# Kernel tuning notes

Hardware: AMD Instinct MI355X
Metric: run time of the kernel (lower is better)

The kernel has to match this reference:

```python
import jax, jax.numpy as jnp
import numpy as np

H = 8            # num_heads
WIN = 128        # num_windows (sliding-window half-width)
B, T, C = 2, 4096, 512


def setup_inputs() -> dict:
    key = jax.random.key(0)
    k1, k2, k3 = jax.random.split(key, 3)
    x = jax.random.normal(k1, (B, T, C), dtype=jnp.float32)
    W_qkv = jax.random.normal(k2, (C, 3 * C), dtype=jnp.float32) * (C ** -0.5)
    W_out = jax.random.normal(k3, (C, C), dtype=jnp.float32) * (C ** -0.5)
    b_out = jnp.zeros((C,), dtype=jnp.float32)
    return {"x": x, "W_qkv": W_qkv, "W_out": W_out, "b_out": b_out}


def reference(x, W_qkv, W_out, b_out):
    Bx, Tx, Cx = x.shape
    hd = Cx // H
    scale = hd ** -0.5
    # qkv projection -> [B, T, 3, H, hd]
    qkv = (x @ W_qkv).reshape(Bx, Tx, 3, H, hd)
    q, k, v = qkv[:, :, 0], qkv[:, :, 1], qkv[:, :, 2]  # each [B, T, H, hd]
    # attention scores [B, H, T, T]
    scores = jnp.einsum('bihd,bjhd->bhij', q, k) * scale
    idx = jnp.arange(Tx)
    band = jnp.abs(idx[:, None] - idx[None, :]) <= WIN  # [T, T] bool
    scores = jnp.where(band[None, None], scores, jnp.float32(-jnp.inf))
    attn = jax.nn.softmax(scores, axis=-1)
    # dropout is identity in eval mode (p handled by config; omitted)
    out = jnp.einsum('bhij,bjhd->bihd', attn, v).reshape(Bx, Tx, Cx)
    return out @ W_out + b_out
```

## Files before the change

kernel.cpp:

```cpp
#include <hip/hip_runtime.h>
#include <stdint.h>

typedef unsigned short ushort_t;
typedef __attribute__((ext_vector_type(8))) __bf16 bf16x8;
typedef __attribute__((ext_vector_type(8))) unsigned short ushortx8;
typedef __attribute__((ext_vector_type(4))) float floatx4;
typedef __attribute__((ext_vector_type(4))) unsigned int uint4v;

__device__ inline ushort_t f2bf(float f) {
  union { float f; unsigned u; } v; v.f = f;
  unsigned r = v.u + 0x7FFFu + ((v.u >> 16) & 1u);
  return (ushort_t)(r >> 16);
}

__device__ inline floatx4 mfma16(bf16x8 a, bf16x8 b, floatx4 c) {
  return __builtin_amdgcn_mfma_f32_16x16x32_bf16(a, b, c, 0, 0, 0);
}

__device__ inline void gload_lds16(const ushort_t* g, ushort_t* l) {
  __builtin_amdgcn_global_load_lds((__attribute__((address_space(1))) void*)(void*)(g),
                                   (__attribute__((address_space(3))) void*)(l),
                                   16, 0, 0);
}

__global__ __launch_bounds__(256)
void k_prep(const float* __restrict__ x, ushort_t* __restrict__ xb,
            const float* __restrict__ Wqkv, ushort_t* __restrict__ wqkvT,
            const float* __restrict__ Wout, ushort_t* __restrict__ woutT) {
  int bx = blockIdx.x, tid = threadIdx.x;
  if (bx < 4096) {
    int i = (bx * 256 + tid) * 4;
    float4 v = *(const float4*)(x + i);
    ushort4 o;
    o.x = f2bf(v.x); o.y = f2bf(v.y); o.z = f2bf(v.z); o.w = f2bf(v.w);
    *(ushort4*)(xb + i) = o;
    return;
  }
  __shared__ float tile[32][33];
  const float* src; ushort_t* dst; int N, id;
  if (bx < 4096 + 768) { id = bx - 4096; src = Wqkv; dst = wqkvT; N = 1536; }
  else                 { id = bx - 4864; src = Wout; dst = woutT; N = 512;  }
  int k0 = (id & 15) * 32, n0 = (id >> 4) * 32;
  int c = tid & 31, r0 = tid >> 5;
#pragma unroll
  for (int i = 0; i < 4; ++i) {
    int r = r0 + i * 8;
    tile[r][c] = src[(size_t)(k0 + r) * N + n0 + c];
  }
  __syncthreads();
#pragma unroll
  for (int i = 0; i < 4; ++i) {
    int r = r0 + i * 8;
    dst[(size_t)(n0 + r) * 512 + k0 + c] = f2bf(tile[c][r]);
  }
}

template <int EPI, int MT>
__global__ __launch_bounds__(256)
void k_gemm_bt(const ushort_t* __restrict__ A, const ushort_t* __restrict__ Bt,
               ushort_t* __restrict__ qd, ushort_t* __restrict__ kd, ushort_t* __restrict__ vd,
               float* __restrict__ outf, const float* __restrict__ bias) {
  constexpr int ABLK = MT / 16;
  constexpr int AISS = ABLK * 2;
  constexpr int TOT  = AISS + 16;
  constexpr int PER  = TOT / 4;
  constexpr int IT   = MT / 32;
  __shared__ __align__(16) ushort_t As[ABLK * 1024];
  __shared__ __align__(16) ushort_t Bs[8 * 1024];
  const int tid = threadIdx.x;
  const int w = tid >> 6, l = tid & 63;
  const int lr = l & 15, lq = l >> 4;
  const int m0 = blockIdx.x * MT, n0 = blockIdx.y * 128;
  const int wm = w >> 1, wn = w & 1;

  floatx4 acc[IT][4];
#pragma unroll
  for (int i = 0; i < IT; ++i)
#pragma unroll
    for (int j = 0; j < 4; ++j) acc[i][j] = (floatx4)0.0f;

  for (int k0 = 0; k0 < 512; k0 += 64) {
#pragma unroll
    for (int i = 0; i < PER; ++i) {
      int idx = w * PER + i;
      if (idx < AISS) {
        int blk = idx >> 1, half = idx & 1;
        gload_lds16(A + (size_t)(m0 + blk * 16 + lr) * 512 + k0 + half * 32 + lq * 8,
                    &As[blk * 1024 + half * 512]);
      } else {
        int j = idx - AISS, blk = j >> 1, half = j & 1;
        gload_lds16(Bt + (size_t)(n0 + blk * 16 + lr) * 512 + k0 + half * 32 + lq * 8,
                    &Bs[blk * 1024 + half * 512]);
      }
    }
    __syncthreads();
#pragma unroll
    for (int half = 0; half < 2; ++half) {
      bf16x8 af[IT], bfr[4];
#pragma unroll
      for (int i = 0; i < IT; ++i)
        af[i] = *(const bf16x8*)&As[(wm * IT + i) * 1024 + half * 512 + l * 8];
#pragma unroll
      for (int j = 0; j < 4; ++j)
        bfr[j] = *(const bf16x8*)&Bs[(wn * 4 + j) * 1024 + half * 512 + l * 8];
#pragma unroll
      for (int i = 0; i < IT; ++i)
#pragma unroll
        for (int j = 0; j < 4; ++j) acc[i][j] = mfma16(af[i], bfr[j], acc[i][j]);
    }
    __syncthreads();
  }

#pragma unroll
  for (int i = 0; i < IT; ++i) {
#pragma unroll
    for (int j = 0; j < 4; ++j) {
      int n = n0 + wn * 64 + j * 16 + lr;
      if (EPI == 0) {
        int which = n >> 9, h = (n >> 6) & 7, d = n & 63;
        ushort_t* dst = (which == 0) ? qd : (which == 1) ? kd : vd;
#pragma unroll
        for (int r = 0; r < 4; ++r) {
          int m = m0 + wm * (IT * 16) + i * 16 + lq * 4 + r;
          int b = m >> 12, t = m & 4095;
          dst[(((size_t)(b * 8 + h)) * 4096 + t) * 64 + d] = f2bf(acc[i][j][r]);
        }
      } else {
        float bv = bias[n];
#pragma unroll
        for (int r = 0; r < 4; ++r) {
          int m = m0 + wm * (IT * 16) + i * 16 + lq * 4 + r;
          outf[(size_t)m * 512 + n] = acc[i][j][r] + bv;
        }
      }
    }
  }
}

__global__ __launch_bounds__(256) void k_transpose_v(const ushort_t* __restrict__ v,
                                                     ushort_t* __restrict__ vt) {
  __shared__ __align__(16) ushort_t lt[64][72];
  int tid = threadIdx.x, w = tid >> 6, l = tid & 63;
  int bh = blockIdx.y, t0 = blockIdx.x * 64;
  int row = w * 16 + (l & 15), ch = (l >> 4) * 16;
  const ushort_t* src = v + ((size_t)bh * 4096 + t0 + row) * 64 + ch;
  *(ushortx8*)&lt[row][ch] = *(const ushortx8*)src;
  *(ushortx8*)&lt[row][ch + 8] = *(const ushortx8*)(src + 8);
  __syncthreads();
  ushortx8 o0, o1;
#pragma unroll
  for (int i = 0; i < 8; ++i) o0[i] = lt[w * 16 + i][l];
#pragma unroll
  for (int i = 0; i < 8; ++i) o1[i] = lt[w * 16 + 8 + i][l];
  ushort_t* dst = vt + ((size_t)bh * 64 + l) * 4096 + t0 + w * 16;
  *(ushortx8*)dst = o0;
  *(ushortx8*)(dst + 8) = o1;
}

__global__ __launch_bounds__(256)
void k_attn(const ushort_t* __restrict__ qa, const ushort_t* __restrict__ ka,
            const ushort_t* __restrict__ vta, ushort_t* __restrict__ ao) {
  __shared__ __align__(16) ushort_t Vs[40 * 512];
  const int tid = threadIdx.x, w = tid >> 6, l = tid & 63;
  const int lr = l & 15, lq = l >> 4;
  const int bh = blockIdx.y, qt0 = blockIdx.x * 64;
  const int qrow = qt0 + w * 16;

  const ushort_t* vbase = vta + (size_t)bh * 64 * 4096;
#pragma unroll
  for (int i = 0; i < 10; ++i) {
    int t = w * 10 + i;
    int kt2 = t >> 2, nt = t & 3;
    int d = nt * 16 + lr;
    int key = qt0 - 128 + kt2 * 32 + lq * 8;
    key = min(max(key, 0), 4088);
    gload_lds16(vbase + (size_t)d * 4096 + key, &Vs[t * 512]);
  }

  const ushort_t* qp = qa + ((size_t)bh * 4096 + qrow + lr) * 64 + lq * 8;
  bf16x8 qf0 = *(const bf16x8*)qp;
  bf16x8 qf1 = *(const bf16x8*)(qp + 32);

  const float C = 0.125f * 1.4426950408889634f;
  uint2 pk[18];
  pk[17].x = 0u; pk[17].y = 0u;
  float ps = 0.f;
#pragma unroll
  for (int kt = 0; kt < 17; ++kt) {
    int kb = qrow - 128 + kt * 16;
    int kc = min(max(kb + lr, 0), 4095);
    const ushort_t* kp = ka + ((size_t)bh * 4096 + kc) * 64 + lq * 8;
    bf16x8 kf0 = *(const bf16x8*)kp;
    bf16x8 kf1 = *(const bf16x8*)(kp + 32);
    floatx4 s = (floatx4)0.0f;
    s = mfma16(kf0, qf0, s);
    s = mfma16(kf1, qf1, s);
    float p[4];
#pragma unroll
    for (int r = 0; r < 4; ++r) {
      int r_rel = kt * 16 + lq * 4 + r;
      int kj = qrow - 128 + r_rel;
      bool ok = (kj >= 0) && (kj < 4096) && (r_rel >= lr) && (r_rel - lr <= 256);
      float e = ok ? exp2f(s[r] * C) : 0.f;
      ps += e;
      p[r] = e;
    }
    pk[kt].x = (unsigned)f2bf(p[0]) | ((unsigned)f2bf(p[1]) << 16);
    pk[kt].y = (unsigned)f2bf(p[2]) | ((unsigned)f2bf(p[3]) << 16);
  }

  ps += __shfl_xor(ps, 16, 64);
  ps += __shfl_xor(ps, 32, 64);
  float inv = __builtin_amdgcn_rcpf(ps);

  __syncthreads();

  floatx4 oacc[4];
#pragma unroll
  for (int nt = 0; nt < 4; ++nt) oacc[nt] = (floatx4)0.0f;
  const int srcA = ((l >> 4) & 1) * 32 + lr;
  const int srcB = srcA + 16;
  const bool selhi = (l & 32) != 0;

#pragma unroll
  for (int kk = 0; kk < 9; ++kk) {
    unsigned e0 = __shfl(pk[2 * kk].x, srcA, 64);
    unsigned e1 = __shfl(pk[2 * kk].y, srcA, 64);
    unsigned e2 = __shfl(pk[2 * kk].x, srcB, 64);
    unsigned e3 = __shfl(pk[2 * kk].y, srcB, 64);
    unsigned o0 = __shfl(pk[2 * kk + 1].x, srcA, 64);
    unsigned o1 = __shfl(pk[2 * kk + 1].y, srcA, 64);
    unsigned o2 = __shfl(pk[2 * kk + 1].x, srcB, 64);
    unsigned o3 = __shfl(pk[2 * kk + 1].y, srcB, 64);
    union { uint4v u; bf16x8 b; } pu;
    pu.u[0] = selhi ? o0 : e0;
    pu.u[1] = selhi ? o1 : e1;
    pu.u[2] = selhi ? o2 : e2;
    pu.u[3] = selhi ? o3 : e3;

    int keyrel = w * 16 + kk * 32 + lq * 8;
    keyrel = min(keyrel, 312);
    int kt2 = keyrel >> 5, seg = (keyrel >> 3) & 3;
    const ushort_t* vsp = &Vs[kt2 * 2048 + seg * 128 + lr * 8];
#pragma unroll
    for (int nt = 0; nt < 4; ++nt) {
      bf16x8 vf = *(const bf16x8*)(vsp + nt * 512);
      oacc[nt] = mfma16(pu.b, vf, oacc[nt]);
    }
  }

  float invr[4];
#pragma unroll
  for (int r = 0; r < 4; ++r) invr[r] = __shfl(inv, lq * 4 + r, 64);

  int b = bh >> 3, h = bh & 7;
#pragma unroll
  for (int nt = 0; nt < 4; ++nt)
#pragma unroll
    for (int r = 0; r < 4; ++r) {
      int t = qrow + lq * 4 + r;
      int col = h * 64 + nt * 16 + lr;
      ao[((size_t)(b * 4096 + t)) * 512 + col] = f2bf(oacc[nt][r] * invr[r]);
    }
}

extern "C" void kernel_launch(void* const* d_in, const int* in_sizes, int n_in,
                              void* d_out, int out_size, void* d_ws, size_t ws_size,
                              hipStream_t stream) {
  const float* x    = (const float*)d_in[0];
  const float* Wqkv = (const float*)d_in[1];
  const float* Wout = (const float*)d_in[2];
  const float* bout = (const float*)d_in[3];
  float* out = (float*)d_out;
  char* ws = (char*)d_ws;
  const size_t MB = 1024 * 1024;

  ushort_t* xb    = (ushort_t*)(ws);
  ushort_t* wqkvT = (ushort_t*)(ws + 8 * MB);
  ushort_t* woutT = (ushort_t*)(ws + 9 * MB + MB/2);
  ushort_t* q     = (ushort_t*)(ws + 10 * MB);
  ushort_t* k     = (ushort_t*)(ws + 18 * MB);
  ushort_t* v     = (ushort_t*)(ws + 26 * MB);
  ushort_t* vt    = (ushort_t*)(ws + 34 * MB);
  ushort_t* ao    = xb;

  k_prep<<<5120, 256, 0, stream>>>(x, xb, Wqkv, wqkvT, Wout, woutT);
  k_gemm_bt<0, 128><<<dim3(64, 12), 256, 0, stream>>>(xb, wqkvT, q, k, v, nullptr, nullptr);
  k_transpose_v<<<dim3(64, 16), 256, 0, stream>>>(v, vt);
  k_attn<<<dim3(64, 16), 256, 0, stream>>>(q, k, vt, ao);
  k_gemm_bt<1, 64><<<dim3(128, 4), 256, 0, stream>>>(ao, woutT, nullptr, nullptr, nullptr, out, bout);
}
```

Before: 156.7 us.

## Fuse V transpose into QKV GEMM epilogue, stage K in LDS, coalesce outputs

The QKV GEMM epilogue now stages its tile through LDS and writes Q/K with 16-byte vector stores. It writes V directly in transposed layout, which removes the separate transpose kernel and the intermediate V buffer. The attention kernel loads its K window into shared memory with async global-to-LDS copies, then reuses the same buffer for V. Attention and output-projection epilogues also go through LDS so their global stores are coalesced. In exchange there are extra barriers, more LDS use and serialized K/V staging in attention.

Measured after the change: 143.8 us. 8.2% less time.

```diff
diff --git a/kernel.cpp b/kernel.cpp
--- a/kernel.cpp
+++ b/kernel.cpp
@@ -55,40 +55,35 @@
   }
 }
 
-template <int EPI, int MT>
 __global__ __launch_bounds__(256)
-void k_gemm_bt(const ushort_t* __restrict__ A, const ushort_t* __restrict__ Bt,
-               ushort_t* __restrict__ qd, ushort_t* __restrict__ kd, ushort_t* __restrict__ vd,
-               float* __restrict__ outf, const float* __restrict__ bias) {
-  constexpr int ABLK = MT / 16;
-  constexpr int AISS = ABLK * 2;
-  constexpr int TOT  = AISS + 16;
-  constexpr int PER  = TOT / 4;
-  constexpr int IT   = MT / 32;
-  __shared__ __align__(16) ushort_t As[ABLK * 1024];
-  __shared__ __align__(16) ushort_t Bs[8 * 1024];
+void k_gemm1(const ushort_t* __restrict__ A, const ushort_t* __restrict__ Bt,
+             ushort_t* __restrict__ qd, ushort_t* __restrict__ kd,
+             ushort_t* __restrict__ vtd) {
+  __shared__ __align__(16) ushort_t smem[17408];
+  ushort_t* As = smem;
+  ushort_t* Bs = smem + 8192;
   const int tid = threadIdx.x;
   const int w = tid >> 6, l = tid & 63;
   const int lr = l & 15, lq = l >> 4;
-  const int m0 = blockIdx.x * MT, n0 = blockIdx.y * 128;
+  const int m0 = blockIdx.x * 128, n0 = blockIdx.y * 128;
   const int wm = w >> 1, wn = w & 1;
 
-  floatx4 acc[IT][4];
-#pragma unroll
-  for (int i = 0; i < IT; ++i)
+  floatx4 acc[4][4];
+#pragma unroll
+  for (int i = 0; i < 4; ++i)
 #pragma unroll
     for (int j = 0; j < 4; ++j) acc[i][j] = (floatx4)0.0f;
 
   for (int k0 = 0; k0 < 512; k0 += 64) {
 #pragma unroll
-    for (int i = 0; i < PER; ++i) {
-      int idx = w * PER + i;
-      if (idx < AISS) {
+    for (int i = 0; i < 8; ++i) {
+      int idx = w * 8 + i;
+      if (idx < 16) {
         int blk = idx >> 1, half = idx & 1;
         gload_lds16(A + (size_t)(m0 + blk * 16 + lr) * 512 + k0 + half * 32 + lq * 8,
                     &As[blk * 1024 + half * 512]);
       } else {
-        int j = idx - AISS, blk = j >> 1, half = j & 1;
+        int j = idx - 16, blk = j >> 1, half = j & 1;
         gload_lds16(Bt + (size_t)(n0 + blk * 16 + lr) * 512 + k0 + half * 32 + lq * 8,
                     &Bs[blk * 1024 + half * 512]);
       }
@@ -96,102 +91,176 @@
     __syncthreads();
 #pragma unroll
     for (int half = 0; half < 2; ++half) {
-      bf16x8 af[IT], bfr[4];
-#pragma unroll
-      for (int i = 0; i < IT; ++i)
-        af[i] = *(const bf16x8*)&As[(wm * IT + i) * 1024 + half * 512 + l * 8];
+      bf16x8 af[4], bfr[4];
+#pragma unroll
+      for (int i = 0; i < 4; ++i)
+        af[i] = *(const bf16x8*)&As[(wm * 4 + i) * 1024 + half * 512 + l * 8];
 #pragma unroll
       for (int j = 0; j < 4; ++j)
         bfr[j] = *(const bf16x8*)&Bs[(wn * 4 + j) * 1024 + half * 512 + l * 8];
 #pragma unroll
-      for (int i = 0; i < IT; ++i)
+      for (int i = 0; i < 4; ++i)
 #pragma unroll
         for (int j = 0; j < 4; ++j) acc[i][j] = mfma16(af[i], bfr[j], acc[i][j]);
     }
     __syncthreads();
   }
 
-#pragma unroll
-  for (int i = 0; i < IT; ++i) {
+  if (blockIdx.y < 8) {
+#pragma unroll
+    for (int i = 0; i < 4; ++i)
+#pragma unroll
+      for (int j = 0; j < 4; ++j) {
+        int col = wn * 64 + j * 16 + lr;
+#pragma unroll
+        for (int r = 0; r < 4; ++r) {
+          int row = wm * 64 + i * 16 + lq * 4 + r;
+          smem[row * 136 + col] = f2bf(acc[i][j][r]);
+        }
+      }
+    __syncthreads();
+#pragma unroll
+    for (int p = 0; p < 8; ++p) {
+      int row = p * 16 + (tid >> 4), c8 = (tid & 15) * 8;
+      ushortx8 vv = *(const ushortx8*)&smem[row * 136 + c8];
+      int n = n0 + c8;
+      ushort_t* dst = (n >> 9) ? kd : qd;
+      int h = (n >> 6) & 7, d = n & 63;
+      int m = m0 + row, b = m >> 12, t = m & 4095;
+      *(ushortx8*)&dst[(((size_t)(b * 8 + h)) * 4096 + t) * 64 + d] = vv;
+    }
+  } else {
+#pragma unroll
+    for (int i = 0; i < 4; ++i)
+#pragma unroll
+      for (int j = 0; j < 4; ++j) {
+        int dcol = wn * 64 + j * 16 + lr;
+        int trow = wm * 64 + i * 16 + lq * 4;
+        ushort4 pv;
+        pv.x = f2bf(acc[i][j][0]); pv.y = f2bf(acc[i][j][1]);
+        pv.z = f2bf(acc[i][j][2]); pv.w = f2bf(acc[i][j][3]);
+        *(ushort4*)&smem[dcol * 136 + trow] = pv;
+      }
+    __syncthreads();
+#pragma unroll
+    for (int p = 0; p < 8; ++p) {
+      int row = p * 16 + (tid >> 4), c8 = (tid & 15) * 8;
+      ushortx8 vv = *(const ushortx8*)&smem[row * 136 + c8];
+      int n = n0 + row, h = (n >> 6) & 7, d = n & 63;
+      int m = m0 + c8, b = m >> 12, t = m & 4095;
+      *(ushortx8*)&vtd[(((size_t)(b * 8 + h)) * 64 + d) * 4096 + t] = vv;
+    }
+  }
+}
+
+__global__ __launch_bounds__(256)
+void k_gemm2(const ushort_t* __restrict__ A, const ushort_t* __restrict__ Bt,
+             float* __restrict__ outf, const float* __restrict__ bias) {
+  __shared__ __align__(16) char smemc[33792];
+  ushort_t* As = (ushort_t*)smemc;
+  ushort_t* Bs = (ushort_t*)(smemc + 8192);
+  float* Cs = (float*)smemc;
+  const int tid = threadIdx.x;
+  const int w = tid >> 6, l = tid & 63;
+  const int lr = l & 15, lq = l >> 4;
+  const int m0 = blockIdx.x * 64, n0 = blockIdx.y * 128;
+  const int wm = w >> 1, wn = w & 1;
+
+  floatx4 acc[2][4];
+#pragma unroll
+  for (int i = 0; i < 2; ++i)
+#pragma unroll
+    for (int j = 0; j < 4; ++j) acc[i][j] = (floatx4)0.0f;
+
+  for (int k0 = 0; k0 < 512; k0 += 64) {
+#pragma unroll
+    for (int i = 0; i < 6; ++i) {
+      int idx = w * 6 + i;
+      if (idx < 8) {
+        int blk = idx >> 1, half = idx & 1;
+        gload_lds16(A + (size_t)(m0 + blk * 16 + lr) * 512 + k0 + half * 32 + lq * 8,
+                    &As[blk * 1024 + half * 512]);
+      } else {
+        int j = idx - 8, blk = j >> 1, half = j & 1;
+        gload_lds16(Bt + (size_t)(n0 + blk * 16 + lr) * 512 + k0 + half * 32 + lq * 8,
+                    &Bs[blk * 1024 + half * 512]);
+      }
+    }
+    __syncthreads();
+#pragma unroll
+    for (int half = 0; half < 2; ++half) {
+      bf16x8 af[2], bfr[4];
+#pragma unroll
+      for (int i = 0; i < 2; ++i)
+        af[i] = *(const bf16x8*)&As[(wm * 2 + i) * 1024 + half * 512 + l * 8];
+#pragma unroll
+      for (int j = 0; j < 4; ++j)
+        bfr[j] = *(const bf16x8*)&Bs[(wn * 4 + j) * 1024 + half * 512 + l * 8];
+#pragma unroll
+      for (int i = 0; i < 2; ++i)
+#pragma unroll
+        for (int j = 0; j < 4; ++j) acc[i][j] = mfma16(af[i], bfr[j], acc[i][j]);
+    }
+    __syncthreads();
+  }
+
+#pragma unroll
+  for (int i = 0; i < 2; ++i)
 #pragma unroll
     for (int j = 0; j < 4; ++j) {
-      int n = n0 + wn * 64 + j * 16 + lr;
-      if (EPI == 0) {
-        int which = n >> 9, h = (n >> 6) & 7, d = n & 63;
-        ushort_t* dst = (which == 0) ? qd : (which == 1) ? kd : vd;
-#pragma unroll
-        for (int r = 0; r < 4; ++r) {
-          int m = m0 + wm * (IT * 16) + i * 16 + lq * 4 + r;
-          int b = m >> 12, t = m & 4095;
-          dst[(((size_t)(b * 8 + h)) * 4096 + t) * 64 + d] = f2bf(acc[i][j][r]);
-        }
-      } else {
-        float bv = bias[n];
-#pragma unroll
-        for (int r = 0; r < 4; ++r) {
-          int m = m0 + wm * (IT * 16) + i * 16 + lq * 4 + r;
-          outf[(size_t)m * 512 + n] = acc[i][j][r] + bv;
-        }
-      }
-    }
-  }
-}
-
-__global__ __launch_bounds__(256) void k_transpose_v(const ushort_t* __restrict__ v,
-                                                     ushort_t* __restrict__ vt) {
-  __shared__ __align__(16) ushort_t lt[64][72];
-  int tid = threadIdx.x, w = tid >> 6, l = tid & 63;
-  int bh = blockIdx.y, t0 = blockIdx.x * 64;
-  int row = w * 16 + (l & 15), ch = (l >> 4) * 16;
-  const ushort_t* src = v + ((size_t)bh * 4096 + t0 + row) * 64 + ch;
-  *(ushortx8*)&lt[row][ch] = *(const ushortx8*)src;
-  *(ushortx8*)&lt[row][ch + 8] = *(const ushortx8*)(src + 8);
-  __syncthreads();
-  ushortx8 o0, o1;
-#pragma unroll
-  for (int i = 0; i < 8; ++i) o0[i] = lt[w * 16 + i][l];
-#pragma unroll
-  for (int i = 0; i < 8; ++i) o1[i] = lt[w * 16 + 8 + i][l];
-  ushort_t* dst = vt + ((size_t)bh * 64 + l) * 4096 + t0 + w * 16;
-  *(ushortx8*)dst = o0;
-  *(ushortx8*)(dst + 8) = o1;
+      int col = wn * 64 + j * 16 + lr;
+      float bv = bias[n0 + col];
+#pragma unroll
+      for (int r = 0; r < 4; ++r) {
+        int row = wm * 32 + i * 16 + lq * 4 + r;
+        Cs[row * 132 + col] = acc[i][j][r] + bv;
+      }
+    }
+  __syncthreads();
+#pragma unroll
+  for (int p = 0; p < 4; ++p) {
+    int row = p * 16 + (tid >> 4), c = (tid & 15) * 8;
+    float4 v0 = *(const float4*)&Cs[row * 132 + c];
+    float4 v1 = *(const float4*)&Cs[row * 132 + c + 4];
+    float* op = &outf[(size_t)(m0 + row) * 512 + n0 + c];
+    *(float4*)op = v0;
+    *(float4*)(op + 4) = v1;
+  }
 }
 
 __global__ __launch_bounds__(256)
 void k_attn(const ushort_t* __restrict__ qa, const ushort_t* __restrict__ ka,
             const ushort_t* __restrict__ vta, ushort_t* __restrict__ ao) {
-  __shared__ __align__(16) ushort_t Vs[40 * 512];
+  __shared__ __align__(16) ushort_t S[20 * 1024];
   const int tid = threadIdx.x, w = tid >> 6, l = tid & 63;
   const int lr = l & 15, lq = l >> 4;
   const int bh = blockIdx.y, qt0 = blockIdx.x * 64;
   const int qrow = qt0 + w * 16;
 
-  const ushort_t* vbase = vta + (size_t)bh * 64 * 4096;
+  const ushort_t* kbase = ka + (size_t)bh * 4096 * 64;
 #pragma unroll
   for (int i = 0; i < 10; ++i) {
-    int t = w * 10 + i;
-    int kt2 = t >> 2, nt = t & 3;
-    int d = nt * 16 + lr;
-    int key = qt0 - 128 + kt2 * 32 + lq * 8;
-    key = min(max(key, 0), 4088);
-    gload_lds16(vbase + (size_t)d * 4096 + key, &Vs[t * 512]);
+    int idx = w * 10 + i, blk = idx >> 1, half = idx & 1;
+    int row = qt0 - 128 + blk * 16 + lr;
+    row = min(max(row, 0), 4095);
+    gload_lds16(kbase + (size_t)row * 64 + half * 32 + lq * 8, &S[blk * 1024 + half * 512]);
   }
 
   const ushort_t* qp = qa + ((size_t)bh * 4096 + qrow + lr) * 64 + lq * 8;
   bf16x8 qf0 = *(const bf16x8*)qp;
   bf16x8 qf1 = *(const bf16x8*)(qp + 32);
 
-  const float C = 0.125f * 1.4426950408889634f;
+  __syncthreads();
+
+  const float Cc = 0.125f * 1.4426950408889634f;
   uint2 pk[18];
   pk[17].x = 0u; pk[17].y = 0u;
   float ps = 0.f;
 #pragma unroll
   for (int kt = 0; kt < 17; ++kt) {
-    int kb = qrow - 128 + kt * 16;
-    int kc = min(max(kb + lr, 0), 4095);
-    const ushort_t* kp = ka + ((size_t)bh * 4096 + kc) * 64 + lq * 8;
+    const ushort_t* kp = &S[(w + kt) * 1024 + l * 8];
     bf16x8 kf0 = *(const bf16x8*)kp;
-    bf16x8 kf1 = *(const bf16x8*)(kp + 32);
+    bf16x8 kf1 = *(const bf16x8*)(kp + 512);
     floatx4 s = (floatx4)0.0f;
     s = mfma16(kf0, qf0, s);
     s = mfma16(kf1, qf1, s);
@@ -201,7 +270,7 @@
       int r_rel = kt * 16 + lq * 4 + r;
       int kj = qrow - 128 + r_rel;
       bool ok = (kj >= 0) && (kj < 4096) && (r_rel >= lr) && (r_rel - lr <= 256);
-      float e = ok ? exp2f(s[r] * C) : 0.f;
+      float e = ok ? exp2f(s[r] * Cc) : 0.f;
       ps += e;
       p[r] = e;
     }
@@ -212,16 +281,26 @@
   ps += __shfl_xor(ps, 16, 64);
   ps += __shfl_xor(ps, 32, 64);
   float inv = __builtin_amdgcn_rcpf(ps);
-
-  __syncthreads();
-
-  floatx4 oacc[4];
-#pragma unroll
-  for (int nt = 0; nt < 4; ++nt) oacc[nt] = (floatx4)0.0f;
+  float invr[4];
+#pragma unroll
+  for (int r = 0; r < 4; ++r) invr[r] = __shfl(inv, lq * 4 + r, 64);
+
+  __syncthreads();
+
+  const ushort_t* vbase = vta + (size_t)bh * 64 * 4096;
+#pragma unroll
+  for (int i = 0; i < 10; ++i) {
+    int t = w * 10 + i, kt2 = t >> 2, nt = t & 3;
+    int d = nt * 16 + lr;
+    int key = qt0 - 128 + kt2 * 32 + lq * 8;
+    key = min(max(key, 0), 4088);
+    gload_lds16(vbase + (size_t)d * 4096 + key, &S[t * 512]);
+  }
+
   const int srcA = ((l >> 4) & 1) * 32 + lr;
   const int srcB = srcA + 16;
   const bool selhi = (l & 32) != 0;
-
+  bf16x8 pu9[9];
 #pragma unroll
   for (int kk = 0; kk < 9; ++kk) {
     unsigned e0 = __shfl(pk[2 * kk].x, srcA, 64);
@@ -237,31 +316,43 @@
     pu.u[1] = selhi ? o1 : e1;
     pu.u[2] = selhi ? o2 : e2;
     pu.u[3] = selhi ? o3 : e3;
-
+    pu9[kk] = pu.b;
+  }
+
+  __syncthreads();
+
+  floatx4 oacc[4];
+#pragma unroll
+  for (int nt = 0; nt < 4; ++nt) oacc[nt] = (floatx4)0.0f;
+#pragma unroll
+  for (int kk = 0; kk < 9; ++kk) {
     int keyrel = w * 16 + kk * 32 + lq * 8;
     keyrel = min(keyrel, 312);
     int kt2 = keyrel >> 5, seg = (keyrel >> 3) & 3;
-    const ushort_t* vsp = &Vs[kt2 * 2048 + seg * 128 + lr * 8];
+    const ushort_t* vsp = &S[kt2 * 2048 + seg * 128 + lr * 8];
 #pragma unroll
     for (int nt = 0; nt < 4; ++nt) {
       bf16x8 vf = *(const bf16x8*)(vsp + nt * 512);
-      oacc[nt] = mfma16(pu.b, vf, oacc[nt]);
-    }
-  }
-
-  float invr[4];
-#pragma unroll
-  for (int r = 0; r < 4; ++r) invr[r] = __shfl(inv, lq * 4 + r, 64);
+      oacc[nt] = mfma16(pu9[kk], vf, oacc[nt]);
+    }
+  }
+
+  __syncthreads();
+
+#pragma unroll
+  for (int nt = 0; nt < 4; ++nt)
+#pragma unroll
+    for (int r = 0; r < 4; ++r)
+      S[(w * 16 + lq * 4 + r) * 72 + nt * 16 + lr] = f2bf(oacc[nt][r] * invr[r]);
+  __syncthreads();
 
   int b = bh >> 3, h = bh & 7;
 #pragma unroll
-  for (int nt = 0; nt < 4; ++nt)
-#pragma unroll
-    for (int r = 0; r < 4; ++r) {
-      int t = qrow + lq * 4 + r;
-      int col = h * 64 + nt * 16 + lr;
-      ao[((size_t)(b * 4096 + t)) * 512 + col] = f2bf(oacc[nt][r] * invr[r]);
-    }
+  for (int p = 0; p < 2; ++p) {
+    int row = p * 32 + (tid >> 3), c8 = (tid & 7) * 8;
+    ushortx8 vv = *(const ushortx8*)&S[row * 72 + c8];
+    *(ushortx8*)&ao[((size_t)(b * 4096 + qt0 + row)) * 512 + h * 64 + c8] = vv;
+  }
 }
 
 extern "C" void kernel_launch(void* const* d_in, const int* in_sizes, int n_in,
@@ -280,13 +371,11 @@
   ushort_t* woutT = (ushort_t*)(ws + 9 * MB + MB/2);
   ushort_t* q     = (ushort_t*)(ws + 10 * MB);
   ushort_t* k     = (ushort_t*)(ws + 18 * MB);
-  ushort_t* v     = (ushort_t*)(ws + 26 * MB);
-  ushort_t* vt    = (ushort_t*)(ws + 34 * MB);
+  ushort_t* vt    = (ushort_t*)(ws + 26 * MB);
   ushort_t* ao    = xb;
 
   k_prep<<<5120, 256, 0, stream>>>(x, xb, Wqkv, wqkvT, Wout, woutT);
-  k_gemm_bt<0, 128><<<dim3(64, 12), 256, 0, stream>>>(xb, wqkvT, q, k, v, nullptr, nullptr);
-  k_transpose_v<<<dim3(64, 16), 256, 0, stream>>>(v, vt);
+  k_gemm1<<<dim3(64, 12), 256, 0, stream>>>(xb, wqkvT, q, k, vt);
   k_attn<<<dim3(64, 16), 256, 0, stream>>>(q, k, vt, ao);
-  k_gemm_bt<1, 64><<<dim3(128, 4), 256, 0, stream>>>(ao, woutT, nullptr, nullptr, nullptr, out, bout);
-}
+  k_gemm2<<<dim3(128, 4), 256, 0, stream>>>(ao, woutT, out, bout);
+}
```
